# Optimization experiments

Hardware: AMD Instinct MI355X
Metric: run time of the kernel (lower is better)

Reference implementation:

```python
import jax, jax.numpy as jnp
import numpy as np

BG_ID = 0
RADIUS = 10
MODE = 'gauss'
LAMBDA_B = 1.0
GAMMA = 0.1
TEMP = 4.0
EPS = 1e-8
BIG = 1e6  # stands in for +inf (no fg in a row/column); BIG**2 is fp32-safe


def setup_inputs() -> dict:
    key = jax.random.key(0)
    k1, k2 = jax.random.split(key)
    B, C, H, W = 4, 19, 256, 256
    return {
        'student_logits': jax.random.normal(k1, (B, C, H, W), jnp.float32),
        'teacher_logits': jax.random.normal(k2, (B, C, H, W), jnp.float32),
    }


def _edt2(fg):
    """Exact squared Euclidean distance transform of (1 - fg):
    distance from each pixel to the nearest foreground pixel.
    Separable algorithm: 1D column pass (two cumulative scans), then
    exact lower-envelope minimization along rows (vectorized brute force).
    fg: bool [B, H, W]. Returns float32 [B, H, W]."""
    B, H, W = fg.shape
    ii = jnp.arange(H, dtype=jnp.float32)[None, :, None]  # row index
    # 1D vertical distance to nearest fg pixel in each column
    d_fwd = ii - jax.lax.cummax(jnp.where(fg, ii, -BIG), axis=1)
    d_bwd = -jax.lax.cummax(jnp.where(fg, -ii, -BIG), axis=1, reverse=True) - ii
    g = jnp.minimum(jnp.minimum(d_fwd, d_bwd), BIG)  # [B,H,W]
    # exact 2D squared EDT: dist2[b,i,j] = min_{j'} (j-j')^2 + g[b,i,j']^2
    jj = jnp.arange(W, dtype=jnp.float32)
    diff2 = (jj[:, None] - jj[None, :]) ** 2  # [W, W']
    dist2 = jnp.min(diff2[None, None, :, :] + (g * g)[:, :, None, :], axis=-1)
    return dist2


def _erode(fg):
    """scipy.ndimage.binary_erosion with 4-connected cross structure and
    border_value=0 (out-of-bounds treated as background)."""
    p = jnp.pad(fg, ((0, 0), (1, 1), (1, 1)))
    return fg & p[:, :-2, 1:-1] & p[:, 2:, 1:-1] & p[:, 1:-1, :-2] & p[:, 1:-1, 2:]


def _weight_map(teacher_logits):
    # argmax of softmax(probs) == argmax of logits (softmax is monotone per-pixel)
    pred = jnp.argmax(teacher_logits, axis=1)  # [B,H,W]
    fg = pred != BG_ID
    dist2 = _edt2(fg)
    dist = jnp.sqrt(dist2)
    mask = (dist <= RADIUS).astype(jnp.float32)
    sigma = RADIUS / 2.0
    if MODE == 'gauss':
        wdist = jnp.exp(-dist2 / (2.0 * sigma * sigma))
    else:
        wdist = jnp.clip(1.0 - dist / RADIUS, 0.0, 1.0)
    wdist = wdist * mask
    boundary = (fg & ~_erode(fg)).astype(jnp.float32)
    # wb = wdist*(1+lambda_b*boundary); final weights = wb*mask_inside
    # (if an image has no fg pixels, dist is huge -> mask==0 -> weights==0,
    #  matching the scipy loop's `continue` which leaves zeros)
    return wdist * (1.0 + LAMBDA_B * boundary) * mask


def reference(student_logits, teacher_logits):
    weight_map = _weight_map(teacher_logits)  # [B,H,W]
    # teacher probs at temperature T (torch computes t_prob_T and t_prob
    # identically twice; computed once here)
    t_prob = jax.nn.softmax(teacher_logits / TEMP, axis=1)
    entropy = -jnp.sum(t_prob * jnp.log(jnp.clip(t_prob, EPS, None)), axis=1)
    ent_max = jnp.max(entropy, axis=(1, 2), keepdims=True)
    conf_factor = GAMMA + (1.0 - GAMMA) * (1.0 - entropy / (ent_max + EPS))
    s_logp = jax.nn.log_softmax(student_logits / TEMP, axis=1)
    kl_per_pixel = jnp.sum(t_prob * (jnp.log(t_prob + EPS) - s_logp), axis=1)
    total_weight = weight_map * conf_factor
    loss = jnp.sum(total_weight * kl_per_pixel) / (jnp.sum(total_weight) + EPS)
    return TEMP * TEMP * loss
```

## Files before the change

kernel.cpp:

```cpp
#include <hip/hip_runtime.h>
#include <math.h>

#define NC   19
#define HH   256
#define WW   256
#define NB   4
#define HW   (HH * WW)
#define NPIX (NB * HW)
#define NQ   (NPIX / 4)
#define CHQ  (HW / 4)
#define CAP2 121.0f

__global__ __launch_bounds__(256) void k_pixel(
    const float4* __restrict__ student, const float4* __restrict__ teacher,
    float4* __restrict__ entropy, float4* __restrict__ kl,
    uchar4* __restrict__ fg, float* __restrict__ bmax)
{
    const int q  = blockIdx.x * 256 + threadIdx.x;
    const int b  = q >> 14;
    const int rq = q & (CHQ - 1);
    const float4* tb = teacher + (size_t)b * NC * CHQ + rq;
    const float4* sb = student + (size_t)b * NC * CHQ + rq;

    float St[4] = {0.f, 0.f, 0.f, 0.f};
    float T1[4] = {0.f, 0.f, 0.f, 0.f};
    float T2[4] = {0.f, 0.f, 0.f, 0.f};
    float Ss[4] = {0.f, 0.f, 0.f, 0.f};
    float tmx[4] = {-INFINITY, -INFINITY, -INFINITY, -INFINITY};
    int   ax[4] = {0, 0, 0, 0};

#pragma unroll
    for (int c = 0; c < NC; ++c) {
        float4 tv4 = tb[(size_t)c * CHQ];
        float4 sv4 = sb[(size_t)c * CHQ];
        float tvl[4] = {tv4.x, tv4.y, tv4.z, tv4.w};
        float svl[4] = {sv4.x, sv4.y, sv4.z, sv4.w};
#pragma unroll
        for (int l = 0; l < 4; ++l) {
            float t = tvl[l], s = svl[l];
            if (t > tmx[l]) { tmx[l] = t; ax[l] = c; }
            float e = __expf(t * 0.25f);
            St[l] += e;
            T1[l] += e * t;
            T2[l] += e * s;
            Ss[l] += __expf(s * 0.25f);
        }
    }

    float4 ent4, kl4;
    uchar4 f4;
    float em = -INFINITY;
#pragma unroll
    for (int l = 0; l < 4; ++l) {
        float rSt = 1.0f / St[l];
        float e = __logf(St[l]) - 0.25f * T1[l] * rSt;
        float k = __logf(Ss[l]) - 0.25f * T2[l] * rSt - e;
        ((float*)&ent4)[l] = e;
        ((float*)&kl4)[l]  = k;
        ((unsigned char*)&f4)[l] = (ax[l] != 0) ? 1 : 0;
        em = fmaxf(em, e);
    }
    entropy[q] = ent4;
    kl[q]      = kl4;
    fg[q]      = f4;

#pragma unroll
    for (int o = 32; o >= 1; o >>= 1) em = fmaxf(em, __shfl_down(em, o, 64));
    __shared__ float red[4];
    int wave = threadIdx.x >> 6, lane = threadIdx.x & 63;
    if (lane == 0) red[wave] = em;
    __syncthreads();
    if (threadIdx.x == 0)
        bmax[blockIdx.x] = fmaxf(fmaxf(red[0], red[1]), fmaxf(red[2], red[3]));
}

#define TS   32
#define HALO 10
#define FW   (TS + 2 * HALO)

__global__ __launch_bounds__(512) void k_tile(
    const unsigned char* __restrict__ fg, const float* __restrict__ entropy,
    const float* __restrict__ kl, const float* __restrict__ bmax,
    double* __restrict__ part)
{
    __shared__ float  fgt[FW][FW];
    __shared__ float  vm[TS][FW];
    __shared__ double snum[8], sden[8];

    const int b   = blockIdx.z;
    const int ti0 = blockIdx.y * TS;
    const int tj0 = blockIdx.x * TS;
    const int tid = threadIdx.x;
    const int wave = tid >> 6, lane = tid & 63;
    const unsigned char* fgb = fg + (size_t)b * HW;

    float m = bmax[(b << 6) + lane];
#pragma unroll
    for (int o = 32; o >= 1; o >>= 1) m = fmaxf(m, __shfl_xor(m, o, 64));
    const float em = m;

    for (int l = tid; l < FW * FW; l += 512) {
        int li = l / FW, lj = l - li * FW;
        int gi = ti0 - HALO + li, gj = tj0 - HALO + lj;
        float v = 0.f;
        if (gi >= 0 && gi < HH && gj >= 0 && gj < WW) v = (float)fgb[gi * WW + gj];
        fgt[li][lj] = v;
    }
    __syncthreads();

    for (int l = tid; l < TS * FW; l += 512) {
        int i = l / FW, jj = l - i * FW;
        float mn = CAP2;
#pragma unroll
        for (int di = -HALO; di <= HALO; ++di) {
            float fv = fgt[HALO + i + di][jj];
            mn = fminf(mn, (float)(di * di) + (1.0f - fv) * 1000.0f);
        }
        vm[i][jj] = mn;
    }
    __syncthreads();

    double num = 0.0, den = 0.0;
#pragma unroll
    for (int k = 0; k < (TS * TS) / 512; ++k) {
        int p = tid + k * 512;
        int i = p >> 5, j = p & (TS - 1);
        float d2 = CAP2;
#pragma unroll
        for (int dj = -HALO; dj <= HALO; ++dj)
            d2 = fminf(d2, (float)(dj * dj) + vm[i][j + HALO + dj]);
        float mask  = (d2 <= 100.0f) ? 1.0f : 0.0f;
        float wdist = __expf(-d2 * 0.02f) * mask;

        float f  = fgt[HALO + i][HALO + j];
        float up = fgt[HALO + i - 1][HALO + j];
        float dn = fgt[HALO + i + 1][HALO + j];
        float lf = fgt[HALO + i][HALO + j - 1];
        float rt = fgt[HALO + i][HALO + j + 1];
        float mn4 = fminf(fminf(up, dn), fminf(lf, rt));
        float boundary = (f != 0.f && mn4 == 0.f) ? 1.0f : 0.0f;

        float w = wdist * (1.0f + boundary) * mask;
        size_t gidx = (size_t)b * HW + (size_t)(ti0 + i) * WW + (tj0 + j);
        float conf = 0.1f + 0.9f * (1.0f - entropy[gidx] / (em + 1e-8f));
        float tw = w * conf;
        num += (double)(tw * kl[gidx]);
        den += (double)tw;
    }

#pragma unroll
    for (int o = 32; o >= 1; o >>= 1) {
        num += __shfl_down(num, o, 64);
        den += __shfl_down(den, o, 64);
    }
    if (lane == 0) { snum[wave] = num; sden[wave] = den; }
    __syncthreads();
    if (tid == 0) {
        double n = 0.0, d = 0.0;
#pragma unroll
        for (int wv = 0; wv < 8; ++wv) { n += snum[wv]; d += sden[wv]; }
        int bid = (blockIdx.z << 6) + (blockIdx.y << 3) + blockIdx.x;
        part[bid * 2 + 0] = n;
        part[bid * 2 + 1] = d;
    }
}

__global__ __launch_bounds__(256) void k_final(
    const double* __restrict__ part, float* __restrict__ out)
{
    const int tid = threadIdx.x;
    double num = part[tid * 2 + 0];
    double den = part[tid * 2 + 1];
#pragma unroll
    for (int o = 32; o >= 1; o >>= 1) {
        num += __shfl_down(num, o, 64);
        den += __shfl_down(den, o, 64);
    }
    __shared__ double snum[4], sden[4];
    int wave = tid >> 6, lane = tid & 63;
    if (lane == 0) { snum[wave] = num; sden[wave] = den; }
    __syncthreads();
    if (tid == 0) {
        num = snum[0] + snum[1] + snum[2] + snum[3];
        den = sden[0] + sden[1] + sden[2] + sden[3];
        out[0] = (float)(16.0 * num / (den + 1e-8));
    }
}

extern "C" void kernel_launch(void* const* d_in, const int* in_sizes, int n_in,
                              void* d_out, int out_size, void* d_ws, size_t ws_size,
                              hipStream_t stream)
{
    const float4* student = (const float4*)d_in[0];
    const float4* teacher = (const float4*)d_in[1];
    float* out = (float*)d_out;

    char* ws = (char*)d_ws;
    double*        part    = (double*)(ws + 0);
    float*         bmax    = (float*)(ws + 8192);
    float4*        entropy = (float4*)(ws + 16384);
    float4*        kl      = (float4*)(ws + 16384 + (size_t)NPIX * 4);
    uchar4*        fg      = (uchar4*)(ws + 16384 + (size_t)NPIX * 8);

    k_pixel<<<NQ / 256, 256, 0, stream>>>(student, teacher, entropy, kl, fg, bmax);
    dim3 g2(WW / TS, HH / TS, NB);
    k_tile<<<g2, 512, 0, stream>>>((const unsigned char*)fg,
                                   (const float*)entropy, (const float*)kl,
                                   bmax, part);
    k_final<<<1, 256, 0, stream>>>(part, out);
}
```

Measured before the change: 85.22 us.

## Process two pixels per thread and interleave entropy/KL into one buffer

The pixel kernel now handles two pixels per thread with float2 loads instead of four with float4. This doubles the number of threads and blocks and lowers register pressure. Entropy and KL are stored interleaved as float2 pairs in one buffer, so the tile kernel fetches both with a single 8-byte load, and the per-block max array grows to match the larger grid. The cost is narrower input loads and more blocks to reduce.

```diff
diff --git a/kernel.cpp b/kernel.cpp
--- a/kernel.cpp
+++ b/kernel.cpp
@@ -7,63 +7,49 @@
 #define NB   4
 #define HW   (HH * WW)
 #define NPIX (NB * HW)
-#define NQ   (NPIX / 4)
-#define CHQ  (HW / 4)
+#define NP2  (NPIX / 2)
+#define CH2  (HW / 2)
 #define CAP2 121.0f
 
 __global__ __launch_bounds__(256) void k_pixel(
-    const float4* __restrict__ student, const float4* __restrict__ teacher,
-    float4* __restrict__ entropy, float4* __restrict__ kl,
-    uchar4* __restrict__ fg, float* __restrict__ bmax)
+    const float2* __restrict__ student, const float2* __restrict__ teacher,
+    float4* __restrict__ ekl, uchar2* __restrict__ fg, float* __restrict__ bmax)
 {
-    const int q  = blockIdx.x * 256 + threadIdx.x;
-    const int b  = q >> 14;
-    const int rq = q & (CHQ - 1);
-    const float4* tb = teacher + (size_t)b * NC * CHQ + rq;
-    const float4* sb = student + (size_t)b * NC * CHQ + rq;
+    const int p2 = blockIdx.x * 256 + threadIdx.x;
+    const int b  = p2 >> 15;
+    const int r2 = p2 & (CH2 - 1);
+    const float2* tp = teacher + (size_t)b * NC * CH2 + r2;
+    const float2* sp = student + (size_t)b * NC * CH2 + r2;
 
-    float St[4] = {0.f, 0.f, 0.f, 0.f};
-    float T1[4] = {0.f, 0.f, 0.f, 0.f};
-    float T2[4] = {0.f, 0.f, 0.f, 0.f};
-    float Ss[4] = {0.f, 0.f, 0.f, 0.f};
-    float tmx[4] = {-INFINITY, -INFINITY, -INFINITY, -INFINITY};
-    int   ax[4] = {0, 0, 0, 0};
-
+    float St0 = 0.f, St1 = 0.f, T10 = 0.f, T11 = 0.f;
+    float T20 = 0.f, T21 = 0.f, Ss0 = 0.f, Ss1 = 0.f;
+    float tm0 = -INFINITY, tm1 = -INFINITY;
+    int ax0 = 0, ax1 = 0;
 #pragma unroll
     for (int c = 0; c < NC; ++c) {
-        float4 tv4 = tb[(size_t)c * CHQ];
-        float4 sv4 = sb[(size_t)c * CHQ];
-        float tvl[4] = {tv4.x, tv4.y, tv4.z, tv4.w};
-        float svl[4] = {sv4.x, sv4.y, sv4.z, sv4.w};
-#pragma unroll
-        for (int l = 0; l < 4; ++l) {
-            float t = tvl[l], s = svl[l];
-            if (t > tmx[l]) { tmx[l] = t; ax[l] = c; }
-            float e = __expf(t * 0.25f);
-            St[l] += e;
-            T1[l] += e * t;
-            T2[l] += e * s;
-            Ss[l] += __expf(s * 0.25f);
-        }
+        float2 tv = tp[(size_t)c * CH2];
+        float2 sv = sp[(size_t)c * CH2];
+        if (tv.x > tm0) { tm0 = tv.x; ax0 = c; }
+        float e0 = __expf(tv.x * 0.25f);
+        St0 += e0; T10 += e0 * tv.x; T20 += e0 * sv.x;
+        Ss0 += __expf(sv.x * 0.25f);
+        if (tv.y > tm1) { tm1 = tv.y; ax1 = c; }
+        float e1 = __expf(tv.y * 0.25f);
+        St1 += e1; T11 += e1 * tv.y; T21 += e1 * sv.y;
+        Ss1 += __expf(sv.y * 0.25f);
     }
+    float r0 = 1.0f / St0, r1 = 1.0f / St1;
+    float e0 = __logf(St0) - 0.25f * T10 * r0;
+    float e1 = __logf(St1) - 0.25f * T11 * r1;
+    float k0 = __logf(Ss0) - 0.25f * T20 * r0 - e0;
+    float k1 = __logf(Ss1) - 0.25f * T21 * r1 - e1;
 
-    float4 ent4, kl4;
-    uchar4 f4;
-    float em = -INFINITY;
-#pragma unroll
-    for (int l = 0; l < 4; ++l) {
-        float rSt = 1.0f / St[l];
-        float e = __logf(St[l]) - 0.25f * T1[l] * rSt;
-        float k = __logf(Ss[l]) - 0.25f * T2[l] * rSt - e;
-        ((float*)&ent4)[l] = e;
-        ((float*)&kl4)[l]  = k;
-        ((unsigned char*)&f4)[l] = (ax[l] != 0) ? 1 : 0;
-        em = fmaxf(em, e);
-    }
-    entropy[q] = ent4;
-    kl[q]      = kl4;
-    fg[q]      = f4;
+    float4 v; v.x = e0; v.y = k0; v.z = e1; v.w = k1;
+    ekl[p2] = v;
+    uchar2 f; f.x = (ax0 != 0) ? 1 : 0; f.y = (ax1 != 0) ? 1 : 0;
+    fg[p2] = f;
 
+    float em = fmaxf(e0, e1);
 #pragma unroll
     for (int o = 32; o >= 1; o >>= 1) em = fmaxf(em, __shfl_down(em, o, 64));
     __shared__ float red[4];
@@ -79,9 +65,8 @@
 #define FW   (TS + 2 * HALO)
 
 __global__ __launch_bounds__(512) void k_tile(
-    const unsigned char* __restrict__ fg, const float* __restrict__ entropy,
-    const float* __restrict__ kl, const float* __restrict__ bmax,
-    double* __restrict__ part)
+    const unsigned char* __restrict__ fg, const float2* __restrict__ ekl,
+    const float* __restrict__ bmax, double* __restrict__ part)
 {
     __shared__ float  fgt[FW][FW];
     __shared__ float  vm[TS][FW];
@@ -94,7 +79,7 @@
     const int wave = tid >> 6, lane = tid & 63;
     const unsigned char* fgb = fg + (size_t)b * HW;
 
-    float m = bmax[(b << 6) + lane];
+    float m = fmaxf(bmax[(b << 7) + lane], bmax[(b << 7) + 64 + lane]);
 #pragma unroll
     for (int o = 32; o >= 1; o >>= 1) m = fmaxf(m, __shfl_xor(m, o, 64));
     const float em = m;
@@ -142,9 +127,10 @@
 
         float w = wdist * (1.0f + boundary) * mask;
         size_t gidx = (size_t)b * HW + (size_t)(ti0 + i) * WW + (tj0 + j);
-        float conf = 0.1f + 0.9f * (1.0f - entropy[gidx] / (em + 1e-8f));
+        float2 ek = ekl[gidx];
+        float conf = 0.1f + 0.9f * (1.0f - ek.x / (em + 1e-8f));
         float tw = w * conf;
-        num += (double)(tw * kl[gidx]);
+        num += (double)(tw * ek.y);
         den += (double)tw;
     }
 
@@ -191,21 +177,18 @@
                               void* d_out, int out_size, void* d_ws, size_t ws_size,
                               hipStream_t stream)
 {
-    const float4* student = (const float4*)d_in[0];
-    const float4* teacher = (const float4*)d_in[1];
+    const float2* student = (const float2*)d_in[0];
+    const float2* teacher = (const float2*)d_in[1];
     float* out = (float*)d_out;
 
     char* ws = (char*)d_ws;
-    double*        part    = (double*)(ws + 0);
-    float*         bmax    = (float*)(ws + 8192);
-    float4*        entropy = (float4*)(ws + 16384);
-    float4*        kl      = (float4*)(ws + 16384 + (size_t)NPIX * 4);
-    uchar4*        fg      = (uchar4*)(ws + 16384 + (size_t)NPIX * 8);
+    double*        part = (double*)(ws + 0);
+    float*         bmax = (float*)(ws + 8192);
+    float4*        ekl  = (float4*)(ws + 16384);
+    unsigned char* fg   = (unsigned char*)(ws + 16384 + (size_t)NPIX * 8);
 
-    k_pixel<<<NQ / 256, 256, 0, stream>>>(student, teacher, entropy, kl, fg, bmax);
+    k_pixel<<<NP2 / 256, 256, 0, stream>>>(student, teacher, ekl, (uchar2*)fg, bmax);
     dim3 g2(WW / TS, HH / TS, NB);
-    k_tile<<<g2, 512, 0, stream>>>((const unsigned char*)fg,
-                                   (const float*)entropy, (const float*)kl,
-                                   bmax, part);
+    k_tile<<<g2, 512, 0, stream>>>(fg, (const float2*)ekl, bmax, part);
     k_final<<<1, 256, 0, stream>>>(part, out);
 }
```

New measurement: 85.59 us. About the same (+0.4%).
